# Optimization experiments

Hardware: AMD Instinct MI355X
Metric: run time of the kernel (lower is better)

## Reference

```python
import jax, jax.numpy as jnp
import numpy as np
import math

B, L, D_IN, D, H, NL, FF = 8, 1024, 32, 512, 8, 6, 64
DK = D // H

def _ln(x, g, b, eps=1e-5):
    m = jnp.mean(x, axis=-1, keepdims=True)
    v = jnp.mean((x - m) ** 2, axis=-1, keepdims=True)
    return (x - m) * jax.lax.rsqrt(v + eps) * g + b

def setup_inputs() -> dict:
    key = jax.random.key(0)
    ks = jax.random.split(key, 32)
    def nrm(k, shape, s=0.02):
        return jax.random.normal(k, shape, jnp.float32) * s
    x = jax.random.normal(ks[0], (B, L, D_IN), jnp.float32)
    mask = jnp.broadcast_to(jnp.tril(jnp.ones((L, L), jnp.int32))[None], (B, L, L))
    obs_time = jnp.arange(B * L, dtype=jnp.float32).reshape(B, L)
    inp = {
        "x": x, "mask": mask, "obs_time": obs_time,
        # embedding MLP: Linear(d_input,d) -> ReLU -> [Dropout] -> LayerNorm -> Linear(d,d)
        "emb_w1": nrm(ks[1], (D_IN, D)), "emb_b1": jnp.zeros((D,), jnp.float32),
        "emb_g": jnp.ones((D,), jnp.float32), "emb_beta": jnp.zeros((D,), jnp.float32),
        "emb_w2": nrm(ks[2], (D, D)), "emb_b2": jnp.zeros((D,), jnp.float32),
        # per-layer stacked params [NL, ...]
        "wq": nrm(ks[3], (NL, D, D)), "wk": nrm(ks[4], (NL, D, D)), "wv": nrm(ks[5], (NL, D, D)),
        "wo": nrm(ks[6], (NL, D, D)), "bo": jnp.zeros((NL, D), jnp.float32),
        "fw1": nrm(ks[7], (NL, D, FF)), "fb1": jnp.zeros((NL, FF), jnp.float32),
        "fw2": nrm(ks[8], (NL, FF, D)), "fb2": jnp.zeros((NL, D), jnp.float32),
        "g1": jnp.ones((NL, D), jnp.float32), "b1": jnp.zeros((NL, D), jnp.float32),
        "g2": jnp.ones((NL, D), jnp.float32), "b2": jnp.zeros((NL, D), jnp.float32),
    }
    return inp

def reference(x, mask, obs_time, emb_w1, emb_b1, emb_g, emb_beta, emb_w2, emb_b2,
              wq, wk, wv, wo, bo, fw1, fb1, fw2, fb2, g1, b1, g2, b2):
    # positional encoding: pe[...,0::2]=sin(t*div), pe[...,1::2]=cos(t*div)
    t = obs_time[..., None]  # [B,L,1]
    div = jnp.exp(jnp.arange(0, D, 2, dtype=jnp.float32) * (-math.log(10000.0) / D))
    pe = jnp.stack([jnp.sin(t * div), jnp.cos(t * div)], axis=-1).reshape(x.shape[0], x.shape[1], D)

    # embedding MLP (dropout = identity at eval)
    h = jax.nn.relu(x @ emb_w1 + emb_b1)
    h = _ln(h, emb_g, emb_beta)
    h = h @ emb_w2 + emb_b2
    h = h + pe

    Bx, Lx = h.shape[0], h.shape[1]
    scale = 1.0 / np.sqrt(DK).astype(np.float32)
    mask4 = (mask == 0)[:, None]  # [B,1,L,L]
    for i in range(NL):
        # self-attention
        q = (h @ wq[i]).reshape(Bx, Lx, H, DK).transpose(0, 2, 1, 3)  # bhld
        k = (h @ wk[i]).reshape(Bx, Lx, H, DK).transpose(0, 2, 1, 3)
        v = (h @ wv[i]).reshape(Bx, Lx, H, DK).transpose(0, 2, 1, 3)
        scores = jnp.einsum('bhqd,bhkd->bhqk', q, k) * scale
        scores = jnp.where(mask4, -jnp.inf, scores)
        attn = jax.nn.softmax(scores, axis=-1)
        o = jnp.einsum('bhqk,bhkd->bhqd', attn, v).transpose(0, 2, 1, 3).reshape(Bx, Lx, D)
        o = o @ wo[i] + bo[i]
        h = _ln(h + o, g1[i], b1[i])
        # feed-forward d -> 64 -> d
        f = jax.nn.relu(h @ fw1[i] + fb1[i]) @ fw2[i] + fb2[i]
        h = _ln(h + f, g2[i], b2[i])
    return h
```

## Files before the change

### kernel.cpp

```cpp
#include <hip/hip_runtime.h>
#include <math.h>

typedef unsigned short u16;
typedef unsigned int   u32;
typedef __bf16 bf16_t;
typedef bf16_t bf16x8 __attribute__((ext_vector_type(8)));
typedef float  f32x4  __attribute__((ext_vector_type(4)));
typedef u16    u16x8  __attribute__((ext_vector_type(8)));
typedef u16    u16x4  __attribute__((ext_vector_type(4)));

#define B_   8
#define L_   1024
#define DIN_ 32
#define D_   512
#define H_   8
#define NL_  6
#define FF_  64
#define M_   (B_*L_)
#define DD_  (D_*D_)

#define PE_COEF (-0.017988946039015984f)
#define SC2     (0.18033688011112042f)

__device__ __forceinline__ u16 f2bf(float f) {
  u32 u = __builtin_bit_cast(u32, f);
  u32 r = (u + 0x7FFFu + ((u >> 16) & 1u)) >> 16;
  return (u16)r;
}
__device__ __forceinline__ u16 f2bf_fast(float f) {
  u32 u = __builtin_bit_cast(u32, f);
  return (u16)((u + 0x8000u) >> 16);
}
__device__ __forceinline__ float bf2f(u16 v) {
  u32 u = ((u32)v) << 16;
  return __builtin_bit_cast(float, u);
}

#define GLOAD_LDS16(gp, lp) \
  __builtin_amdgcn_global_load_lds((const __attribute__((address_space(1))) u32*)(gp), \
                                   (__attribute__((address_space(3))) u32*)(lp), 16, 0, 0)

__device__ __forceinline__ float block_reduce_sum(float v, float* smem4) {
  #pragma unroll
  for (int off = 32; off > 0; off >>= 1) v += __shfl_down(v, off, 64);
  int wid = threadIdx.x >> 6;
  __syncthreads();
  if ((threadIdx.x & 63) == 0) smem4[wid] = v;
  __syncthreads();
  return smem4[0] + smem4[1] + smem4[2] + smem4[3];
}

__global__ __launch_bounds__(256) void transpose_k(const float* __restrict__ W, u16* __restrict__ Wt,
                                                   int K, int N, size_t in_zs, size_t out_zs) {
  __shared__ float tile[32][33];
  size_t mi = (size_t)blockIdx.z * in_zs;
  size_t mo = (size_t)blockIdx.z * out_zs;
  int k0 = blockIdx.y * 32, n0 = blockIdx.x * 32;
  int tx = threadIdx.x & 31, ty = threadIdx.x >> 5;
  #pragma unroll
  for (int i = 0; i < 4; ++i)
    tile[ty + i*8][tx] = W[mi + (size_t)(k0 + ty + i*8)*N + n0 + tx];
  __syncthreads();
  #pragma unroll
  for (int i = 0; i < 4; ++i)
    Wt[mo + (size_t)(n0 + ty + i*8)*K + k0 + tx] = f2bf(tile[tx][ty + i*8]);
}

__global__ __launch_bounds__(256) void emb1_ln_kernel(const float* __restrict__ x, const float* __restrict__ W1,
                               const float* __restrict__ b1, const float* __restrict__ g,
                               const float* __restrict__ beta, u16* __restrict__ outb) {
  __shared__ float xs[DIN_];
  __shared__ float red[4];
  int m = blockIdx.x;
  int tid = threadIdx.x;
  if (tid < DIN_) xs[tid] = x[m*DIN_ + tid];
  __syncthreads();
  float v[2];
  #pragma unroll
  for (int r = 0; r < 2; ++r) {
    int n = tid + r*256;
    float acc = b1[n];
    #pragma unroll
    for (int k = 0; k < DIN_; ++k) acc += xs[k] * W1[k*D_ + n];
    v[r] = fmaxf(acc, 0.f);
  }
  float mean = block_reduce_sum(v[0] + v[1], red) * (1.f/D_);
  float d0 = v[0] - mean, d1 = v[1] - mean;
  float var = block_reduce_sum(d0*d0 + d1*d1, red) * (1.f/D_);
  float rstd = rsqrtf(var + 1e-5f);
  outb[(size_t)m*D_ + tid]       = f2bf(d0*rstd*g[tid]       + beta[tid]);
  outb[(size_t)m*D_ + tid + 256] = f2bf(d1*rstd*g[tid + 256] + beta[tid + 256]);
}

__global__ __launch_bounds__(256) void add_ln_kernel(const float* __restrict__ hin, const u16* __restrict__ res,
                              const float* __restrict__ g, const float* __restrict__ b,
                              float* __restrict__ outf, u16* __restrict__ outb) {
  __shared__ float red[4];
  int m = blockIdx.x;
  int tid = threadIdx.x;
  float v0 = hin[(size_t)m*D_ + tid]       + bf2f(res[(size_t)m*D_ + tid]);
  float v1 = hin[(size_t)m*D_ + tid + 256] + bf2f(res[(size_t)m*D_ + tid + 256]);
  float mean = block_reduce_sum(v0 + v1, red) * (1.f/D_);
  float d0 = v0 - mean, d1 = v1 - mean;
  float var = block_reduce_sum(d0*d0 + d1*d1, red) * (1.f/D_);
  float rstd = rsqrtf(var + 1e-5f);
  float o0 = d0*rstd*g[tid]       + b[tid];
  float o1 = d1*rstd*g[tid + 256] + b[tid + 256];
  outf[(size_t)m*D_ + tid]       = o0;
  outf[(size_t)m*D_ + tid + 256] = o1;
  outb[(size_t)m*D_ + tid]       = f2bf(o0);
  outb[(size_t)m*D_ + tid + 256] = f2bf(o1);
}

template<int BM, int BN, int EPI, bool WF, bool WB>
__global__ __launch_bounds__(256) void mgemm(const u16* __restrict__ A, const u16* __restrict__ Bt,
                            const float* __restrict__ bias, const float* __restrict__ extra,
                            float* __restrict__ Cf, u16* __restrict__ Cb,
                            int M, int N, int K) {
  __shared__ __align__(16) u16 As[2][BM*32];
  __shared__ __align__(16) u16 Bs[2][BN*32];
  const int WR = BM/2, WC = BN/2, MR = WR/16, NR = WC/16;
  int nx = gridDim.x;
  int nwg = nx * gridDim.y;
  int flat = blockIdx.y * nx + blockIdx.x;
  int wid = (flat & 7) * (nwg >> 3) + (flat >> 3);
  int bm = (wid / nx) * BM, bn = (wid % nx) * BN;
  int tid = threadIdx.x, w = tid >> 6, l = tid & 63;
  int wr = w >> 1, wc = w & 1;
  int lq = l & 15, lg = l >> 4;
  f32x4 acc[MR][NR];
  #pragma unroll
  for (int m = 0; m < MR; ++m)
    #pragma unroll
    for (int n = 0; n < NR; ++n) acc[m][n] = f32x4{0.f,0.f,0.f,0.f};

  int srow = w*16 + (l >> 2);
  int scol = (l & 3)*8;

  #pragma unroll
  for (int i = 0; i < BM/64; ++i)
    GLOAD_LDS16(A + (size_t)(bm + i*64 + srow)*K + scol, &As[0][i*2048 + w*512]);
  #pragma unroll
  for (int i = 0; i < BN/64; ++i)
    GLOAD_LDS16(Bt + (size_t)(bn + i*64 + srow)*K + scol, &Bs[0][i*2048 + w*512]);

  int nk = K >> 5;
  #pragma unroll 1
  for (int t = 0; t < nk; ++t) {
    int buf = t & 1;
    __syncthreads();
    if (t + 1 < nk) {
      int k0 = (t + 1) << 5;
      #pragma unroll
      for (int i = 0; i < BM/64; ++i)
        GLOAD_LDS16(A + (size_t)(bm + i*64 + srow)*K + k0 + scol, &As[buf^1][i*2048 + w*512]);
      #pragma unroll
      for (int i = 0; i < BN/64; ++i)
        GLOAD_LDS16(Bt + (size_t)(bn + i*64 + srow)*K + k0 + scol, &Bs[buf^1][i*2048 + w*512]);
    }
    bf16x8 af[MR], bfr[NR];
    #pragma unroll
    for (int m = 0; m < MR; ++m)
      af[m] = *(const bf16x8*)&As[buf][(wr*WR + m*16 + lq)*32 + lg*8];
    #pragma unroll
    for (int n = 0; n < NR; ++n)
      bfr[n] = *(const bf16x8*)&Bs[buf][(wc*WC + n*16 + lq)*32 + lg*8];
    #pragma unroll
    for (int m = 0; m < MR; ++m)
      #pragma unroll
      for (int n = 0; n < NR; ++n)
        acc[m][n] = __builtin_amdgcn_mfma_f32_16x16x32_bf16(af[m], bfr[n], acc[m][n], 0, 0, 0);
  }

  #pragma unroll
  for (int m = 0; m < MR; ++m) {
    #pragma unroll
    for (int n = 0; n < NR; ++n) {
      #pragma unroll
      for (int r = 0; r < 4; ++r) {
        int row = bm + wr*WR + m*16 + lg*4 + r;
        int col = bn + wc*WC + n*16 + lq;
        float v = acc[m][n][r];
        if (EPI & 1) v += bias[col];
        if (EPI & 2) v = fmaxf(v, 0.f);
        if (EPI & 4) {
          float fr  = __expf((float)(col & ~1) * PE_COEF);
          float arg = extra[row] * fr;
          v += (col & 1) ? cosf(arg) : sinf(arg);
        }
        if (WF) Cf[(size_t)row*N + col] = v;
        if (WB) Cb[(size_t)row*N + col] = f2bf(v);
      }
    }
  }
}

#define QS_ 1536
__global__ __launch_bounds__(256) void attn_kernel(const u16* __restrict__ Q, const u16* __restrict__ Kp,
                                                   const u16* __restrict__ V, u16* __restrict__ O) {
  __shared__ __align__(16) u16 Ks[2][64*72];
  __shared__ __align__(16) u16 Vt[2][64*72];
  __shared__ __align__(16) u16 Ps[4][16*72];
  int flat = blockIdx.y * 8 + blockIdx.x;
  int wid  = (flat & 7) * 64 + (flat >> 3);
  int pair = wid & 7, bh = wid >> 3;
  int b = bh >> 3, hh = bh & 7;
  int rowbase = b * L_, col0 = hh * 64;
  int tid = threadIdx.x, w = tid >> 6, l = tid & 63;
  int lq = l & 15, lg = l >> 4;

  int krow = tid >> 3, kseg = tid & 7;
  int vg = tid >> 5, vd2 = (tid & 31) * 2;

  u16x8 kr0, kr1;
  u32 vr[8];
  u16x8 oc16;
  #pragma unroll
  for (int i = 0; i < 8; ++i) oc16[i] = 0x3F80u;
  const bf16x8 onesA = __builtin_bit_cast(bf16x8, oc16);

  #define LOADKV(t) { \
    kr0 = *(const u16x8*)&Kp[(size_t)(rowbase + (t)*64 + krow)*QS_ + col0 + kseg*8]; \
    kr1 = *(const u16x8*)&Kp[(size_t)(rowbase + (t)*64 + krow + 32)*QS_ + col0 + kseg*8]; \
    _Pragma("unroll") \
    for (int i_ = 0; i_ < 8; ++i_) \
      vr[i_] = *(const u32*)&V[(size_t)(rowbase + (t)*64 + vg*8 + i_)*QS_ + col0 + vd2]; }

  LOADKV(0);

  #pragma unroll 1
  for (int half = 0; half < 2; ++half) {
    int qt = half ? (15 - pair) : pair;
    int qrow = rowbase + qt*64 + w*16 + lq;
    bf16x8 qa0 = *(const bf16x8*)&Q[(size_t)qrow*QS_ + col0 + lg*8];
    bf16x8 qa1 = *(const bf16x8*)&Q[(size_t)qrow*QS_ + col0 + 32 + lg*8];
    float m_s[4];
    f32x4 o[4], o4;
    #pragma unroll
    for (int r = 0; r < 4; ++r) m_s[r] = -1e30f;
    #pragma unroll
    for (int n = 0; n < 4; ++n) o[n] = f32x4{0.f,0.f,0.f,0.f};
    o4 = f32x4{0.f,0.f,0.f,0.f};

    #pragma unroll 1
    for (int kt = 0; kt <= qt; ++kt) {
      int buf = kt & 1;
      __syncthreads();
      *(u16x8*)&Ks[buf][krow*72 + kseg*8]        = kr0;
      *(u16x8*)&Ks[buf][(krow + 32)*72 + kseg*8] = kr1;
      {
        u16x8 vlo, vhi;
        #pragma unroll
        for (int i = 0; i < 8; ++i) { vlo[i] = (u16)(vr[i] & 0xffffu); vhi[i] = (u16)(vr[i] >> 16); }
        *(u16x8*)&Vt[buf][vd2*72 + vg*8]     = vlo;
        *(u16x8*)&Vt[buf][(vd2+1)*72 + vg*8] = vhi;
      }
      __syncthreads();
      int nt = (kt < qt) ? (kt + 1) : (half == 0 ? 0 : -1);
      if (nt >= 0) LOADKV(nt);

      f32x4 t4[4];
      #pragma unroll
      for (int f = 0; f < 4; ++f) {
        bf16x8 k0 = *(const bf16x8*)&Ks[buf][(f*16 + lq)*72 + lg*8];
        bf16x8 k1 = *(const bf16x8*)&Ks[buf][(f*16 + lq)*72 + 32 + lg*8];
        f32x4 z = f32x4{0.f,0.f,0.f,0.f};
        z = __builtin_amdgcn_mfma_f32_16x16x32_bf16(qa0, k0, z, 0, 0, 0);
        z = __builtin_amdgcn_mfma_f32_16x16x32_bf16(qa1, k1, z, 0, 0, 0);
        #pragma unroll
        for (int r = 0; r < 4; ++r) t4[f][r] = z[r] * SC2;
      }
      if (kt == qt) {
        #pragma unroll
        for (int f = 0; f < 4; ++f) {
          int kvg = f*16 + lq;
          #pragma unroll
          for (int r = 0; r < 4; ++r)
            if (kvg > w*16 + lg*4 + r) t4[f][r] = -1e30f;
        }
      }
      float tm[4];
      bool need = false;
      #pragma unroll
      for (int r = 0; r < 4; ++r) {
        float v = fmaxf(fmaxf(t4[0][r], t4[1][r]), fmaxf(t4[2][r], t4[3][r]));
        v = fmaxf(v, __shfl_xor(v, 1));
        v = fmaxf(v, __shfl_xor(v, 2));
        v = fmaxf(v, __shfl_xor(v, 4));
        v = fmaxf(v, __shfl_xor(v, 8));
        tm[r] = v;
        need = need || (v > m_s[r]);
      }
      if (__any(need)) {
        float corr[4];
        #pragma unroll
        for (int r = 0; r < 4; ++r) {
          float mn = fmaxf(m_s[r], tm[r]);
          corr[r] = __builtin_amdgcn_exp2f(m_s[r] - mn);
          m_s[r] = mn;
        }
        int bsrc = (lq >> 2)*16 + lq;
        float c0 = __shfl(corr[0], bsrc);
        float c1 = __shfl(corr[1], bsrc);
        float c2 = __shfl(corr[2], bsrc);
        float c3 = __shfl(corr[3], bsrc);
        float cb = (lq & 2) ? ((lq & 1) ? c3 : c2) : ((lq & 1) ? c1 : c0);
        #pragma unroll
        for (int n = 0; n < 4; ++n)
          #pragma unroll
          for (int r = 0; r < 4; ++r) o[n][r] *= cb;
        #pragma unroll
        for (int r = 0; r < 4; ++r) o4[r] *= cb;
      }
      #pragma unroll
      for (int r = 0; r < 4; ++r) {
        int prow = (lg*4 + r)*72;
        Ps[w][prow + lq]      = f2bf_fast(__builtin_amdgcn_exp2f(t4[0][r] - m_s[r]));
        Ps[w][prow + 16 + lq] = f2bf_fast(__builtin_amdgcn_exp2f(t4[1][r] - m_s[r]));
        Ps[w][prow + 32 + lq] = f2bf_fast(__builtin_amdgcn_exp2f(t4[2][r] - m_s[r]));
        Ps[w][prow + 48 + lq] = f2bf_fast(__builtin_amdgcn_exp2f(t4[3][r] - m_s[r]));
      }
      bf16x8 pB0 = *(const bf16x8*)&Ps[w][lq*72 + lg*8];
      bf16x8 pB1 = *(const bf16x8*)&Ps[w][lq*72 + 32 + lg*8];
      o4 = __builtin_amdgcn_mfma_f32_16x16x32_bf16(onesA, pB0, o4, 0, 0, 0);
      o4 = __builtin_amdgcn_mfma_f32_16x16x32_bf16(onesA, pB1, o4, 0, 0, 0);
      #pragma unroll
      for (int n = 0; n < 4; ++n) {
        bf16x8 vA0 = *(const bf16x8*)&Vt[buf][(n*16 + lq)*72 + lg*8];
        bf16x8 vA1 = *(const bf16x8*)&Vt[buf][(n*16 + lq)*72 + 32 + lg*8];
        o[n] = __builtin_amdgcn_mfma_f32_16x16x32_bf16(vA0, pB0, o[n], 0, 0, 0);
        o[n] = __builtin_amdgcn_mfma_f32_16x16x32_bf16(vA1, pB1, o[n], 0, 0, 0);
      }
    }
    float inv = 1.f / o4[0];
    #pragma unroll
    for (int n = 0; n < 4; ++n) {
      u16x4 pk;
      #pragma unroll
      for (int r = 0; r < 4; ++r) pk[r] = f2bf(o[n][r] * inv);
      *(u16x4*)&O[(size_t)(rowbase + qt*64 + w*16 + lq)*D_ + col0 + n*16 + lg*4] = pk;
    }
  }
  #undef LOADKV
}

extern "C" void kernel_launch(void* const* d_in, const int* in_sizes, int n_in,
                              void* d_out, int out_size, void* d_ws, size_t ws_size,
                              hipStream_t stream) {
  (void)in_sizes; (void)n_in; (void)out_size; (void)ws_size;
  const float* x      = (const float*)d_in[0];
  const float* obs    = (const float*)d_in[2];
  const float* emb_w1 = (const float*)d_in[3];
  const float* emb_b1 = (const float*)d_in[4];
  const float* emb_g  = (const float*)d_in[5];
  const float* emb_be = (const float*)d_in[6];
  const float* emb_w2 = (const float*)d_in[7];
  const float* emb_b2 = (const float*)d_in[8];
  const float* wq  = (const float*)d_in[9];
  const float* wk  = (const float*)d_in[10];
  const float* wv  = (const float*)d_in[11];
  const float* wo  = (const float*)d_in[12];
  const float* bo  = (const float*)d_in[13];
  const float* fw1 = (const float*)d_in[14];
  const float* fb1 = (const float*)d_in[15];
  const float* fw2 = (const float*)d_in[16];
  const float* fb2 = (const float*)d_in[17];
  const float* g1  = (const float*)d_in[18];
  const float* b1  = (const float*)d_in[19];
  const float* g2  = (const float*)d_in[20];
  const float* b2  = (const float*)d_in[21];
  float* out = (float*)d_out;

  float* hf  = (float*)d_ws;
  u16* hb    = (u16*)(hf + (size_t)M_*D_);
  u16* qkvb  = hb + (size_t)M_*D_;
  u16* ob    = qkvb + (size_t)M_*3*D_;
  u16* ofb   = ob + (size_t)M_*D_;
  u16* fhb   = ofb + (size_t)M_*D_;
  u16* qkvt  = fhb + (size_t)M_*FF_;
  u16* wot   = qkvt + (size_t)18*DD_;
  u16* ew2t  = wot + (size_t)6*DD_;
  u16* fw1t  = ew2t + (size_t)DD_;
  u16* fw2t  = fw1t + (size_t)6*D_*FF_;

  transpose_k<<<dim3(16,16,6), 256, 0, stream>>>(wq, qkvt,          512, 512, DD_, 3*(size_t)DD_);
  transpose_k<<<dim3(16,16,6), 256, 0, stream>>>(wk, qkvt + DD_,    512, 512, DD_, 3*(size_t)DD_);
  transpose_k<<<dim3(16,16,6), 256, 0, stream>>>(wv, qkvt + 2*DD_,  512, 512, DD_, 3*(size_t)DD_);
  transpose_k<<<dim3(16,16,6), 256, 0, stream>>>(wo, wot,           512, 512, DD_, DD_);
  transpose_k<<<dim3(16,16,1), 256, 0, stream>>>(emb_w2, ew2t,      512, 512, DD_, DD_);
  transpose_k<<<dim3(2,16,6),  256, 0, stream>>>(fw1, fw1t,         512,  64, (size_t)D_*FF_, (size_t)D_*FF_);
  transpose_k<<<dim3(16,2,6),  256, 0, stream>>>(fw2, fw2t,          64, 512, (size_t)D_*FF_, (size_t)D_*FF_);

  emb1_ln_kernel<<<M_, 256, 0, stream>>>(x, emb_w1, emb_b1, emb_g, emb_be, ob);
  mgemm<128,128,5,true,true><<<dim3(4,64), 256, 0, stream>>>(ob, ew2t, emb_b2, obs, hf, hb, M_, D_, D_);

  for (int i = 0; i < NL_; ++i) {
    mgemm<128,128,0,false,true><<<dim3(12,64), 256, 0, stream>>>(hb, qkvt + (size_t)i*3*DD_,
        nullptr, nullptr, nullptr, qkvb, M_, 3*D_, D_);
    attn_kernel<<<dim3(8, B_*H_), 256, 0, stream>>>(qkvb, qkvb + D_, qkvb + 2*D_, ob);
    mgemm<128,128,1,false,true><<<dim3(4,64), 256, 0, stream>>>(ob, wot + (size_t)i*DD_,
        bo + i*D_, nullptr, nullptr, ofb, M_, D_, D_);
    add_ln_kernel<<<M_, 256, 0, stream>>>(hf, ofb, g1 + i*D_, b1 + i*D_, hf, hb);
    mgemm<64,64,3,false,true><<<dim3(1,128), 256, 0, stream>>>(hb, fw1t + (size_t)i*D_*FF_,
        fb1 + i*FF_, nullptr, nullptr, fhb, M_, FF_, D_);
    mgemm<128,128,1,false,true><<<dim3(4,64), 256, 0, stream>>>(fhb, fw2t + (size_t)i*D_*FF_,
        fb2 + i*D_, nullptr, nullptr, ofb, M_, D_, FF_);
    add_ln_kernel<<<M_, 256, 0, stream>>>(hf, ofb, g2 + i*D_, b2 + i*D_,
        (i == NL_-1) ? out : hf, hb);
  }
}
```

Measured before the change: 866.1 us.

## Triple-buffer GEMM LDS pipeline with vmcnt waits; raise priority around attention MFMAs

The GEMM kernel moves from double to triple buffering of its A/B LDS tiles. Loads are issued two k-steps ahead, and each step waits on a partial vmcnt instead of a full barrier plus drain, so global-to-LDS traffic overlaps more with MFMA work. The attention kernel wraps its QK and PV MFMA sections in s_setprio to favour the matrix-issuing waves. The extra buffer raises LDS use per block and may lower occupancy. The hand-written waitcnt counts depend on how many loads each thread issues per stage.

```diff
diff --git a/kernel.cpp b/kernel.cpp
--- a/kernel.cpp
+++ b/kernel.cpp
@@ -117,8 +117,10 @@
                             const float* __restrict__ bias, const float* __restrict__ extra,
                             float* __restrict__ Cf, u16* __restrict__ Cb,
                             int M, int N, int K) {
-  __shared__ __align__(16) u16 As[2][BM*32];
-  __shared__ __align__(16) u16 Bs[2][BN*32];
+  constexpr int NBUF = 3;
+  constexpr int LPT = BM/64 + BN/64;
+  __shared__ __align__(16) u16 As[NBUF][BM*32];
+  __shared__ __align__(16) u16 Bs[NBUF][BN*32];
   const int WR = BM/2, WC = BN/2, MR = WR/16, NR = WC/16;
   int nx = gridDim.x;
   int nwg = nx * gridDim.y;
@@ -137,39 +139,49 @@
   int srow = w*16 + (l >> 2);
   int scol = (l & 3)*8;
 
-  #pragma unroll
-  for (int i = 0; i < BM/64; ++i)
-    GLOAD_LDS16(A + (size_t)(bm + i*64 + srow)*K + scol, &As[0][i*2048 + w*512]);
-  #pragma unroll
-  for (int i = 0; i < BN/64; ++i)
-    GLOAD_LDS16(Bt + (size_t)(bn + i*64 + srow)*K + scol, &Bs[0][i*2048 + w*512]);
+  auto stage = [&](int t, int bi) {
+    int k0 = t << 5;
+    #pragma unroll
+    for (int i = 0; i < BM/64; ++i)
+      GLOAD_LDS16(A + (size_t)(bm + i*64 + srow)*K + k0 + scol, &As[bi][i*2048 + w*512]);
+    #pragma unroll
+    for (int i = 0; i < BN/64; ++i)
+      GLOAD_LDS16(Bt + (size_t)(bn + i*64 + srow)*K + k0 + scol, &Bs[bi][i*2048 + w*512]);
+  };
 
   int nk = K >> 5;
+  stage(0, 0);
+  if (nk > 1) stage(1, 1);
+  int bi = 0;
   #pragma unroll 1
   for (int t = 0; t < nk; ++t) {
-    int buf = t & 1;
-    __syncthreads();
     if (t + 1 < nk) {
-      int k0 = (t + 1) << 5;
-      #pragma unroll
-      for (int i = 0; i < BM/64; ++i)
-        GLOAD_LDS16(A + (size_t)(bm + i*64 + srow)*K + k0 + scol, &As[buf^1][i*2048 + w*512]);
-      #pragma unroll
-      for (int i = 0; i < BN/64; ++i)
-        GLOAD_LDS16(Bt + (size_t)(bn + i*64 + srow)*K + k0 + scol, &Bs[buf^1][i*2048 + w*512]);
+      if constexpr (LPT == 2)      asm volatile("s_waitcnt vmcnt(2)" ::: "memory");
+      else if constexpr (LPT == 3) asm volatile("s_waitcnt vmcnt(3)" ::: "memory");
+      else if constexpr (LPT == 4) asm volatile("s_waitcnt vmcnt(4)" ::: "memory");
+      else                         asm volatile("s_waitcnt vmcnt(0)" ::: "memory");
+    } else {
+      asm volatile("s_waitcnt vmcnt(0)" ::: "memory");
+    }
+    __builtin_amdgcn_s_barrier();
+    __builtin_amdgcn_sched_barrier(0);
+    if (t + 2 < nk) {
+      int b2 = bi + 2; if (b2 >= NBUF) b2 -= NBUF;
+      stage(t + 2, b2);
     }
     bf16x8 af[MR], bfr[NR];
     #pragma unroll
     for (int m = 0; m < MR; ++m)
-      af[m] = *(const bf16x8*)&As[buf][(wr*WR + m*16 + lq)*32 + lg*8];
+      af[m] = *(const bf16x8*)&As[bi][(wr*WR + m*16 + lq)*32 + lg*8];
     #pragma unroll
     for (int n = 0; n < NR; ++n)
-      bfr[n] = *(const bf16x8*)&Bs[buf][(wc*WC + n*16 + lq)*32 + lg*8];
+      bfr[n] = *(const bf16x8*)&Bs[bi][(wc*WC + n*16 + lq)*32 + lg*8];
     #pragma unroll
     for (int m = 0; m < MR; ++m)
       #pragma unroll
       for (int n = 0; n < NR; ++n)
         acc[m][n] = __builtin_amdgcn_mfma_f32_16x16x32_bf16(af[m], bfr[n], acc[m][n], 0, 0, 0);
+    bi = (bi + 1 == NBUF) ? 0 : bi + 1;
   }
 
   #pragma unroll
@@ -260,6 +272,7 @@
       if (nt >= 0) LOADKV(nt);
 
       f32x4 t4[4];
+      __builtin_amdgcn_s_setprio(1);
       #pragma unroll
       for (int f = 0; f < 4; ++f) {
         bf16x8 k0 = *(const bf16x8*)&Ks[buf][(f*16 + lq)*72 + lg*8];
@@ -270,6 +283,7 @@
         #pragma unroll
         for (int r = 0; r < 4; ++r) t4[f][r] = z[r] * SC2;
       }
+      __builtin_amdgcn_s_setprio(0);
       if (kt == qt) {
         #pragma unroll
         for (int f = 0; f < 4; ++f) {
@@ -322,6 +336,7 @@
       }
       bf16x8 pB0 = *(const bf16x8*)&Ps[w][lq*72 + lg*8];
       bf16x8 pB1 = *(const bf16x8*)&Ps[w][lq*72 + 32 + lg*8];
+      __builtin_amdgcn_s_setprio(1);
       o4 = __builtin_amdgcn_mfma_f32_16x16x32_bf16(onesA, pB0, o4, 0, 0, 0);
       o4 = __builtin_amdgcn_mfma_f32_16x16x32_bf16(onesA, pB1, o4, 0, 0, 0);
       #pragma unroll
@@ -331,6 +346,7 @@
         o[n] = __builtin_amdgcn_mfma_f32_16x16x32_bf16(vA0, pB0, o[n], 0, 0, 0);
         o[n] = __builtin_amdgcn_mfma_f32_16x16x32_bf16(vA1, pB1, o[n], 0, 0, 0);
       }
+      __builtin_amdgcn_s_setprio(0);
     }
     float inv = 1.f / o4[0];
     #pragma unroll
```

New measurement: 848.3 us. 1.02x faster.
